# Optimization experiments

Measured on AMD Instinct MI355X. Metric: run time of the kernel, lower is better.

Reference implementation:

```python
import jax, jax.numpy as jnp
import numpy as np

N_NODES = 10000
N_EDGES = 640000
IN_CH = 128
OUT_CH = 128


def setup_inputs() -> dict:
    key = jax.random.key(0)
    k1, k2, k3, k4 = jax.random.split(key, 4)
    x = jax.random.normal(k1, (N_NODES, IN_CH), dtype=jnp.float32)
    edge_index = jax.random.randint(k2, (2, N_EDGES), 0, N_NODES, dtype=jnp.int64)
    # nn.Linear(2*in_channels, out_channels): weight [out, 2*in], bias [out]
    bound = 1.0 / np.sqrt(2 * IN_CH)
    W = jax.random.uniform(k3, (OUT_CH, 2 * IN_CH), dtype=jnp.float32, minval=-bound, maxval=bound)
    b = jax.random.uniform(k4, (OUT_CH,), dtype=jnp.float32, minval=-bound, maxval=bound)
    return {"x": x, "W": W, "b": b, "edge_index": edge_index}


def reference(x, W, b, edge_index):
    # PyG convention: edge_index[0] = source j, edge_index[1] = target i
    src, dst = edge_index[0], edge_index[1]
    x_i = x[dst]                      # [E, C] target features
    x_j = x[src]                      # [E, C] source features
    feat = jnp.concatenate([x_i, x_j - x_i], axis=-1)  # [E, 2C]
    msg = feat @ W.T + b              # [E, out]
    out = jax.ops.segment_max(msg, dst, num_segments=x.shape[0])  # [N, out]
    # isolated nodes: PyG scatter-max yields 0, segment_max yields -inf
    return jnp.where(jnp.isfinite(out), out, 0.0)
```

## Files before the change

### kernel.cpp

```cpp
#include <hip/hip_runtime.h>
#include <math.h>

#define N_CH 128
#define NB_MAX 512
#define BIN_CHUNK 2048
#define BIN_T 512

__global__ __launch_bounds__(256) void prep_kernel(const float* __restrict__ W,
                                                   float* __restrict__ V1,
                                                   float* __restrict__ V2,
                                                   int* __restrict__ binCount,
                                                   int nb) {
    int i = blockIdx.x * 256 + threadIdx.x;
    if (i < N_CH * N_CH) {
        int k = i >> 7, o = i & 127;
        float w1 = W[o * 256 + k];
        float w2 = W[o * 256 + 128 + k];
        V1[i] = w1 - w2;
        V2[i] = w2;
    }
    if (i < nb) binCount[i] = 0;
}

__global__ __launch_bounds__(256) void gemm_kernel(const float* __restrict__ x,
                                                   const float* __restrict__ V1,
                                                   const float* __restrict__ V2,
                                                   const float* __restrict__ bias,
                                                   float* __restrict__ A,
                                                   unsigned short* __restrict__ Bh,
                                                   int n_nodes) {
    __shared__ float xs[32][N_CH];
    const int n0 = blockIdx.x * 32;
    const int tid = threadIdx.x;

    if (n0 + 32 <= n_nodes) {
        const float4* xg = (const float4*)(x + (size_t)n0 * N_CH);
        float4* xsv = (float4*)&xs[0][0];
        #pragma unroll
        for (int i = 0; i < 4; ++i) xsv[tid + i * 256] = xg[tid + i * 256];
    } else {
        for (int i = tid; i < 32 * N_CH; i += 256) {
            int n = n0 + (i >> 7);
            (&xs[0][0])[i] = (n < n_nodes) ? x[(size_t)n * N_CH + (i & 127)] : 0.f;
        }
    }
    __syncthreads();

    const int o  = tid & 127;
    const int nh = tid >> 7;
    const float bo = bias[o];
    float acc1[16], acc2[16];
    #pragma unroll
    for (int i = 0; i < 16; ++i) { acc1[i] = 0.f; acc2[i] = 0.f; }

    const float* xrow = &xs[nh * 16][0];
    for (int k4 = 0; k4 < N_CH; k4 += 4) {
        float w1[4], w2[4];
        #pragma unroll
        for (int j = 0; j < 4; ++j) {
            w1[j] = V1[(k4 + j) * N_CH + o];
            w2[j] = V2[(k4 + j) * N_CH + o];
        }
        #pragma unroll
        for (int i = 0; i < 16; ++i) {
            float4 xv = *(const float4*)&xrow[i * N_CH + k4];
            acc1[i] = fmaf(xv.x, w1[0], acc1[i]); acc2[i] = fmaf(xv.x, w2[0], acc2[i]);
            acc1[i] = fmaf(xv.y, w1[1], acc1[i]); acc2[i] = fmaf(xv.y, w2[1], acc2[i]);
            acc1[i] = fmaf(xv.z, w1[2], acc1[i]); acc2[i] = fmaf(xv.z, w2[2], acc2[i]);
            acc1[i] = fmaf(xv.w, w1[3], acc1[i]); acc2[i] = fmaf(xv.w, w2[3], acc2[i]);
        }
    }

    #pragma unroll
    for (int i = 0; i < 16; ++i) {
        int n = n0 + nh * 16 + i;
        if (n < n_nodes) {
            A[(size_t)n * N_CH + o] = acc1[i] + bo;
            unsigned int bits = __float_as_uint(acc2[i]);
            unsigned int r = (bits + 0x7FFFu + ((bits >> 16) & 1u)) >> 16;
            Bh[(size_t)n * N_CH + o] = (unsigned short)r;
        }
    }
}

__global__ __launch_bounds__(256) void bhist_kernel(const int* __restrict__ dst,
                                                    int* __restrict__ binCount,
                                                    int n_edges, int nb) {
    __shared__ int h[NB_MAX];
    const int tid = threadIdx.x;
    for (int i = tid; i < nb; i += 256) h[i] = 0;
    __syncthreads();
    const int base = blockIdx.x * BIN_CHUNK;
    const int cnt = min(BIN_CHUNK, n_edges - base);
    for (int j = tid; j < cnt; j += 256)
        atomicAdd(&h[dst[base + j] >> 5], 1);
    __syncthreads();
    for (int i = tid; i < nb; i += 256)
        if (h[i]) atomicAdd(&binCount[i], h[i]);
}

__global__ __launch_bounds__(512) void bscan_kernel(const int* __restrict__ binCount,
                                                    int* __restrict__ binOff,
                                                    int* __restrict__ binCursor,
                                                    int nb) {
    __shared__ int t[512];
    const int tid = threadIdx.x;
    int v = (tid < nb) ? binCount[tid] : 0;
    t[tid] = v;
    __syncthreads();
    #pragma unroll
    for (int off = 1; off < 512; off <<= 1) {
        int u = (tid >= off) ? t[tid - off] : 0;
        __syncthreads();
        t[tid] += u;
        __syncthreads();
    }
    if (tid < nb) {
        int excl = t[tid] - v;
        binOff[tid] = excl;
        binCursor[tid] = excl;
    }
    if (tid == 0) binOff[nb] = t[nb - 1];
}

__global__ __launch_bounds__(BIN_T) void bin_kernel(const int* __restrict__ src,
                                                    const int* __restrict__ dst,
                                                    int* __restrict__ binCursor,
                                                    unsigned int* __restrict__ binned,
                                                    int n_edges, int nb) {
    __shared__ unsigned int   lpk[BIN_CHUNK];
    __shared__ unsigned short lbk[BIN_CHUNK];
    __shared__ int sc[512];
    __shared__ int lhist[NB_MAX], lexcl[NB_MAX], lcur[NB_MAX], bbase[NB_MAX];

    const int tid = threadIdx.x;
    const int base = blockIdx.x * BIN_CHUNK;
    const int cnt = min(BIN_CHUNK, n_edges - base);

    for (int i = tid; i < nb; i += BIN_T) lhist[i] = 0;
    __syncthreads();

    unsigned int vreg[BIN_CHUNK / BIN_T];
    unsigned short breg[BIN_CHUNK / BIN_T];
    int nloc = 0;
    for (int j = tid; j < cnt; j += BIN_T) {
        int s = src[base + j];
        int d = dst[base + j];
        int b = d >> 5;
        vreg[nloc] = ((unsigned int)(d & 31) << 14) | (unsigned int)s;
        breg[nloc] = (unsigned short)b;
        ++nloc;
        atomicAdd(&lhist[b], 1);
    }
    __syncthreads();

    int v = (tid < nb) ? lhist[tid] : 0;
    sc[tid] = v;
    __syncthreads();
    #pragma unroll
    for (int off = 1; off < 512; off <<= 1) {
        int u = (tid >= off) ? sc[tid - off] : 0;
        __syncthreads();
        sc[tid] += u;
        __syncthreads();
    }
    if (tid < nb) {
        int excl = sc[tid] - v;
        lexcl[tid] = excl;
        lcur[tid] = excl;
    }
    __syncthreads();

    for (int k = 0; k < nloc; ++k) {
        int b = breg[k];
        int p = atomicAdd(&lcur[b], 1);
        lpk[p] = vreg[k];
        lbk[p] = (unsigned short)b;
    }
    __syncthreads();

    for (int b = tid; b < nb; b += BIN_T) {
        int c = lhist[b];
        if (c) bbase[b] = atomicAdd(&binCursor[b], c);
    }
    __syncthreads();

    for (int i = tid; i < cnt; i += BIN_T) {
        int b = lbk[i];
        binned[bbase[b] + (i - lexcl[b])] = lpk[i];
    }
}

__global__ __launch_bounds__(256) void build_kernel(const unsigned int* __restrict__ binned,
                                                    const int* __restrict__ binOff,
                                                    int* __restrict__ offsets,
                                                    int* __restrict__ eidx,
                                                    int n_nodes, int nb) {
    __shared__ int lhist[32], lexcl[33], lcur[32];
    const int b = blockIdx.x;
    const int tid = threadIdx.x;
    const int rbeg = binOff[b], rend = binOff[b + 1];

    if (tid < 32) { lhist[tid] = 0; lcur[tid] = 0; }
    __syncthreads();
    for (int i = rbeg + tid; i < rend; i += 256)
        atomicAdd(&lhist[binned[i] >> 14], 1);
    __syncthreads();
    if (tid == 0) {
        int s = 0;
        for (int k = 0; k < 32; ++k) { lexcl[k] = s; s += lhist[k]; }
        lexcl[32] = s;
    }
    __syncthreads();
    if (tid < 32) {
        int n = b * 32 + tid;
        if (n < n_nodes) offsets[n] = rbeg + lexcl[tid];
    }
    if (b == nb - 1 && tid == 0) offsets[n_nodes] = rend;
    for (int i = rbeg + tid; i < rend; i += 256) {
        unsigned int w = binned[i];
        int d5 = (int)(w >> 14);
        int r = atomicAdd(&lcur[d5], 1);
        eidx[rbeg + lexcl[d5] + r] = (int)(w & 16383u);
    }
}

__global__ __launch_bounds__(256) void gather_kernel(
        const float* __restrict__ A,
        const uint4* __restrict__ Bh4,
        const int* __restrict__ offsets,
        const int* __restrict__ eidx,
        float* __restrict__ out,
        int n_nodes) {
    __shared__ int sidx[4][64];
    const int g = threadIdx.x >> 6;
    const int l = threadIdx.x & 63;
    const int n = blockIdx.x * 4 + g;
    if (n >= n_nodes) return;
    const int beg = offsets[n], end = offsets[n + 1];

    const int sub = l >> 4;
    const int col = l & 15;

    float mlo[4][4], mhi[4][4];
    #pragma unroll
    for (int s = 0; s < 4; ++s)
        #pragma unroll
        for (int u = 0; u < 4; ++u) { mlo[s][u] = -INFINITY; mhi[s][u] = -INFINITY; }

    for (int base = beg; base < end; base += 64) {
        int p = base + l;
        if (p < end) sidx[g][l] = eidx[p];
        int cnt = min(64, end - base);
        int q = 0;
        for (; q + 16 <= cnt; q += 16) {
            int e[4];
            #pragma unroll
            for (int s = 0; s < 4; ++s) e[s] = sidx[g][q + 4 * s + sub];
            uint4 w[4];
            #pragma unroll
            for (int s = 0; s < 4; ++s) w[s] = Bh4[(size_t)e[s] * 16 + col];
            #pragma unroll
            for (int s = 0; s < 4; ++s) {
                mlo[s][0] = fmaxf(mlo[s][0], __uint_as_float(w[s].x << 16));
                mhi[s][0] = fmaxf(mhi[s][0], __uint_as_float(w[s].x & 0xFFFF0000u));
                mlo[s][1] = fmaxf(mlo[s][1], __uint_as_float(w[s].y << 16));
                mhi[s][1] = fmaxf(mhi[s][1], __uint_as_float(w[s].y & 0xFFFF0000u));
                mlo[s][2] = fmaxf(mlo[s][2], __uint_as_float(w[s].z << 16));
                mhi[s][2] = fmaxf(mhi[s][2], __uint_as_float(w[s].z & 0xFFFF0000u));
                mlo[s][3] = fmaxf(mlo[s][3], __uint_as_float(w[s].w << 16));
                mhi[s][3] = fmaxf(mhi[s][3], __uint_as_float(w[s].w & 0xFFFF0000u));
            }
        }
        for (; q < cnt; q += 4) {
            int r = q + sub;
            if (r < cnt) {
                int e = sidx[g][r];
                uint4 w = Bh4[(size_t)e * 16 + col];
                mlo[0][0] = fmaxf(mlo[0][0], __uint_as_float(w.x << 16));
                mhi[0][0] = fmaxf(mhi[0][0], __uint_as_float(w.x & 0xFFFF0000u));
                mlo[0][1] = fmaxf(mlo[0][1], __uint_as_float(w.y << 16));
                mhi[0][1] = fmaxf(mhi[0][1], __uint_as_float(w.y & 0xFFFF0000u));
                mlo[0][2] = fmaxf(mlo[0][2], __uint_as_float(w.z << 16));
                mhi[0][2] = fmaxf(mhi[0][2], __uint_as_float(w.z & 0xFFFF0000u));
                mlo[0][3] = fmaxf(mlo[0][3], __uint_as_float(w.w << 16));
                mhi[0][3] = fmaxf(mhi[0][3], __uint_as_float(w.w & 0xFFFF0000u));
            }
        }
    }

    float lo[4], hi[4];
    #pragma unroll
    for (int u = 0; u < 4; ++u) {
        lo[u] = fmaxf(fmaxf(mlo[0][u], mlo[1][u]), fmaxf(mlo[2][u], mlo[3][u]));
        hi[u] = fmaxf(fmaxf(mhi[0][u], mhi[1][u]), fmaxf(mhi[2][u], mhi[3][u]));
    }
    #pragma unroll
    for (int u = 0; u < 4; ++u) {
        lo[u] = fmaxf(lo[u], __shfl_xor(lo[u], 16, 64));
        hi[u] = fmaxf(hi[u], __shfl_xor(hi[u], 16, 64));
        lo[u] = fmaxf(lo[u], __shfl_xor(lo[u], 32, 64));
        hi[u] = fmaxf(hi[u], __shfl_xor(hi[u], 32, 64));
    }

    if (sub == 0) {
        float r8[8];
        if (end > beg) {
            const float4* Arow = (const float4*)(A + (size_t)n * N_CH + col * 8);
            float4 a0 = Arow[0], a1 = Arow[1];
            r8[0] = a0.x + lo[0]; r8[1] = a0.y + hi[0];
            r8[2] = a0.z + lo[1]; r8[3] = a0.w + hi[1];
            r8[4] = a1.x + lo[2]; r8[5] = a1.y + hi[2];
            r8[6] = a1.z + lo[3]; r8[7] = a1.w + hi[3];
        } else {
            #pragma unroll
            for (int i = 0; i < 8; ++i) r8[i] = 0.f;
        }
        float4* orow = (float4*)(out + (size_t)n * N_CH + col * 8);
        orow[0] = make_float4(r8[0], r8[1], r8[2], r8[3]);
        orow[1] = make_float4(r8[4], r8[5], r8[6], r8[7]);
    }
}

extern "C" void kernel_launch(void* const* d_in, const int* in_sizes, int n_in,
                              void* d_out, int out_size, void* d_ws, size_t ws_size,
                              hipStream_t stream) {
    const float* x = (const float*)d_in[0];
    const float* W = (const float*)d_in[1];
    const float* b = (const float*)d_in[2];
    const int*   ei = (const int*)d_in[3];

    const int n_nodes = in_sizes[0] / N_CH;
    const int n_edges = in_sizes[3] / 2;
    const int nb = (n_nodes + 31) >> 5;
    const int* src = ei;
    const int* dst = ei + n_edges;
    float* out = (float*)d_out;

    char* ws = (char*)d_ws;
    size_t off = 0;
    auto alloc = [&](size_t bytes) -> void* {
        void* p = ws + off;
        off += (bytes + 255) & ~(size_t)255;
        return p;
    };
    float* V1        = (float*)alloc((size_t)N_CH * N_CH * 4);
    float* V2        = (float*)alloc((size_t)N_CH * N_CH * 4);
    float* A         = (float*)alloc((size_t)n_nodes * N_CH * 4);
    unsigned short* Bh = (unsigned short*)alloc((size_t)n_nodes * N_CH * 2);
    int*   binCount  = (int*)alloc((size_t)nb * 4);
    int*   binOff    = (int*)alloc((size_t)(nb + 1) * 4);
    int*   binCursor = (int*)alloc((size_t)nb * 4);
    unsigned int* binned = (unsigned int*)alloc((size_t)n_edges * 4);
    int*   offsets   = (int*)alloc((size_t)(n_nodes + 1) * 4);
    int*   eidx      = (int*)alloc((size_t)n_edges * 4);
    (void)ws_size; (void)n_in; (void)out_size;

    const int nbin_blocks = (n_edges + BIN_CHUNK - 1) / BIN_CHUNK;

    prep_kernel <<<(N_CH * N_CH + 255) / 256, 256, 0, stream>>>(W, V1, V2, binCount, nb);
    gemm_kernel <<<(n_nodes + 31) / 32, 256, 0, stream>>>(x, V1, V2, b, A, Bh, n_nodes);
    bhist_kernel<<<nbin_blocks, 256, 0, stream>>>(dst, binCount, n_edges, nb);
    bscan_kernel<<<1, 512, 0, stream>>>(binCount, binOff, binCursor, nb);
    bin_kernel  <<<nbin_blocks, BIN_T, 0, stream>>>(src, dst, binCursor, binned, n_edges, nb);
    build_kernel<<<nb, 256, 0, stream>>>(binned, binOff, offsets, eidx, n_nodes, nb);
    gather_kernel<<<(n_nodes + 3) / 4, 256, 0, stream>>>(A, (const uint4*)Bh, offsets, eidx, out, n_nodes);
}
```

Baseline: 141.9 us.

## Replace binned CSR build with per-node histogram fused into GEMM and atomic scatter

Removes the two-level bin/build CSR construction (bhist, bscan, bin, build kernels). A per-node degree histogram is now fused into the GEMM kernel, with a last-block-done pattern doing the prefix scan inside the same launch. A simple global-atomic scatter then fills eidx. This cuts launch count and intermediate traffic, but the scan now runs on a single block and the scatter uses contended global atomics. Edge order within each node also becomes nondeterministic, which is harmless for a max reduction.

```diff
diff --git a/kernel.cpp b/kernel.cpp
--- a/kernel.cpp
+++ b/kernel.cpp
@@ -2,15 +2,13 @@
 #include <math.h>
 
 #define N_CH 128
-#define NB_MAX 512
-#define BIN_CHUNK 2048
-#define BIN_T 512
 
 __global__ __launch_bounds__(256) void prep_kernel(const float* __restrict__ W,
                                                    float* __restrict__ V1,
                                                    float* __restrict__ V2,
-                                                   int* __restrict__ binCount,
-                                                   int nb) {
+                                                   int* __restrict__ nodeCount,
+                                                   int* __restrict__ done,
+                                                   int n_nodes) {
     int i = blockIdx.x * 256 + threadIdx.x;
     if (i < N_CH * N_CH) {
         int k = i >> 7, o = i & 127;
@@ -19,209 +17,143 @@
         V1[i] = w1 - w2;
         V2[i] = w2;
     }
-    if (i < nb) binCount[i] = 0;
-}
-
-__global__ __launch_bounds__(256) void gemm_kernel(const float* __restrict__ x,
-                                                   const float* __restrict__ V1,
-                                                   const float* __restrict__ V2,
-                                                   const float* __restrict__ bias,
-                                                   float* __restrict__ A,
-                                                   unsigned short* __restrict__ Bh,
-                                                   int n_nodes) {
-    __shared__ float xs[32][N_CH];
-    const int n0 = blockIdx.x * 32;
+    int total = gridDim.x * 256;
+    for (int j = i; j < n_nodes; j += total) nodeCount[j] = 0;
+    if (i == 0) *done = 0;
+}
+
+__global__ __launch_bounds__(256) void gemmhist_kernel(
+        const float* __restrict__ x,
+        const float* __restrict__ V1,
+        const float* __restrict__ V2,
+        const float* __restrict__ bias,
+        const int* __restrict__ dst,
+        float* __restrict__ A,
+        unsigned short* __restrict__ Bh,
+        int* __restrict__ nodeCount,
+        int* __restrict__ done,
+        int* __restrict__ offsets,
+        int* __restrict__ cursor,
+        int n_nodes, int n_edges, int ec) {
+    __shared__ float xs[16][N_CH];
+    __shared__ int ps[256];
+    __shared__ int isLast;
     const int tid = threadIdx.x;
-
-    if (n0 + 32 <= n_nodes) {
-        const float4* xg = (const float4*)(x + (size_t)n0 * N_CH);
-        float4* xsv = (float4*)&xs[0][0];
+    const int bid = blockIdx.x;
+
+    {
+        const int base = bid * ec;
+        const int cnt = min(ec, n_edges - base);
+        for (int j = tid; j < cnt; j += 256)
+            atomicAdd(&nodeCount[dst[base + j]], 1);
+    }
+
+    const int n0 = bid * 16;
+    if (n0 < n_nodes) {
+        if (n0 + 16 <= n_nodes) {
+            const float4* xg = (const float4*)(x + (size_t)n0 * N_CH);
+            float4* xsv = (float4*)&xs[0][0];
+            xsv[tid] = xg[tid];
+            xsv[tid + 256] = xg[tid + 256];
+        } else {
+            for (int i = tid; i < 16 * N_CH; i += 256) {
+                int n = n0 + (i >> 7);
+                (&xs[0][0])[i] = (n < n_nodes) ? x[(size_t)n * N_CH + (i & 127)] : 0.f;
+            }
+        }
+        __syncthreads();
+
+        const int o  = tid & 127;
+        const int nh = tid >> 7;
+        const float bo = bias[o];
+        float acc1[8], acc2[8];
         #pragma unroll
-        for (int i = 0; i < 4; ++i) xsv[tid + i * 256] = xg[tid + i * 256];
+        for (int i = 0; i < 8; ++i) { acc1[i] = 0.f; acc2[i] = 0.f; }
+
+        const float* xrow = &xs[nh * 8][0];
+        for (int k4 = 0; k4 < N_CH; k4 += 4) {
+            float w1[4], w2[4];
+            #pragma unroll
+            for (int j = 0; j < 4; ++j) {
+                w1[j] = V1[(k4 + j) * N_CH + o];
+                w2[j] = V2[(k4 + j) * N_CH + o];
+            }
+            #pragma unroll
+            for (int i = 0; i < 8; ++i) {
+                float4 xv = *(const float4*)&xrow[i * N_CH + k4];
+                acc1[i] = fmaf(xv.x, w1[0], acc1[i]); acc2[i] = fmaf(xv.x, w2[0], acc2[i]);
+                acc1[i] = fmaf(xv.y, w1[1], acc1[i]); acc2[i] = fmaf(xv.y, w2[1], acc2[i]);
+                acc1[i] = fmaf(xv.z, w1[2], acc1[i]); acc2[i] = fmaf(xv.z, w2[2], acc2[i]);
+                acc1[i] = fmaf(xv.w, w1[3], acc1[i]); acc2[i] = fmaf(xv.w, w2[3], acc2[i]);
+            }
+        }
+
+        #pragma unroll
+        for (int i = 0; i < 8; ++i) {
+            int n = n0 + nh * 8 + i;
+            if (n < n_nodes) {
+                A[(size_t)n * N_CH + o] = acc1[i] + bo;
+                unsigned int bits = __float_as_uint(acc2[i]);
+                unsigned int r = (bits + 0x7FFFu + ((bits >> 16) & 1u)) >> 16;
+                Bh[(size_t)n * N_CH + o] = (unsigned short)r;
+            }
+        }
+    }
+
+    __threadfence();
+    __syncthreads();
+    if (tid == 0) isLast = (atomicAdd(done, 1) == (int)gridDim.x - 1) ? 1 : 0;
+    __syncthreads();
+    if (!isLast) return;
+
+    const int npt = (n_nodes + 255) >> 8;
+    const int beg = tid * npt;
+    int s = 0;
+    for (int k = 0; k < npt; ++k) {
+        int idx = beg + k;
+        if (idx < n_nodes) s += atomicAdd(&nodeCount[idx], 0);
+    }
+    ps[tid] = s;
+    __syncthreads();
+    #pragma unroll
+    for (int off = 1; off < 256; off <<= 1) {
+        int u = (tid >= off) ? ps[tid - off] : 0;
+        __syncthreads();
+        ps[tid] += u;
+        __syncthreads();
+    }
+    int run = ps[tid] - s;
+    for (int k = 0; k < npt; ++k) {
+        int idx = beg + k;
+        if (idx < n_nodes) {
+            int c = atomicAdd(&nodeCount[idx], 0);
+            offsets[idx] = run;
+            cursor[idx]  = run;
+            run += c;
+        }
+    }
+    if (tid == 255) offsets[n_nodes] = ps[255];
+}
+
+__global__ __launch_bounds__(256) void scatter_kernel(const int* __restrict__ src,
+                                                      const int* __restrict__ dst,
+                                                      int* __restrict__ cursor,
+                                                      int* __restrict__ eidx,
+                                                      int n_edges) {
+    const int g = blockIdx.x * 256 + threadIdx.x;
+    const int base = g * 4;
+    if (base + 4 <= n_edges) {
+        int4 s4 = *(const int4*)(src + base);
+        int4 d4 = *(const int4*)(dst + base);
+        int p0 = atomicAdd(&cursor[d4.x], 1); eidx[p0] = s4.x;
+        int p1 = atomicAdd(&cursor[d4.y], 1); eidx[p1] = s4.y;
+        int p2 = atomicAdd(&cursor[d4.z], 1); eidx[p2] = s4.z;
+        int p3 = atomicAdd(&cursor[d4.w], 1); eidx[p3] = s4.w;
     } else {
-        for (int i = tid; i < 32 * N_CH; i += 256) {
-            int n = n0 + (i >> 7);
-            (&xs[0][0])[i] = (n < n_nodes) ? x[(size_t)n * N_CH + (i & 127)] : 0.f;
-        }
-    }
-    __syncthreads();
-
-    const int o  = tid & 127;
-    const int nh = tid >> 7;
-    const float bo = bias[o];
-    float acc1[16], acc2[16];
-    #pragma unroll
-    for (int i = 0; i < 16; ++i) { acc1[i] = 0.f; acc2[i] = 0.f; }
-
-    const float* xrow = &xs[nh * 16][0];
-    for (int k4 = 0; k4 < N_CH; k4 += 4) {
-        float w1[4], w2[4];
-        #pragma unroll
-        for (int j = 0; j < 4; ++j) {
-            w1[j] = V1[(k4 + j) * N_CH + o];
-            w2[j] = V2[(k4 + j) * N_CH + o];
-        }
-        #pragma unroll
-        for (int i = 0; i < 16; ++i) {
-            float4 xv = *(const float4*)&xrow[i * N_CH + k4];
-            acc1[i] = fmaf(xv.x, w1[0], acc1[i]); acc2[i] = fmaf(xv.x, w2[0], acc2[i]);
-            acc1[i] = fmaf(xv.y, w1[1], acc1[i]); acc2[i] = fmaf(xv.y, w2[1], acc2[i]);
-            acc1[i] = fmaf(xv.z, w1[2], acc1[i]); acc2[i] = fmaf(xv.z, w2[2], acc2[i]);
-            acc1[i] = fmaf(xv.w, w1[3], acc1[i]); acc2[i] = fmaf(xv.w, w2[3], acc2[i]);
-        }
-    }
-
-    #pragma unroll
-    for (int i = 0; i < 16; ++i) {
-        int n = n0 + nh * 16 + i;
-        if (n < n_nodes) {
-            A[(size_t)n * N_CH + o] = acc1[i] + bo;
-            unsigned int bits = __float_as_uint(acc2[i]);
-            unsigned int r = (bits + 0x7FFFu + ((bits >> 16) & 1u)) >> 16;
-            Bh[(size_t)n * N_CH + o] = (unsigned short)r;
-        }
-    }
-}
-
-__global__ __launch_bounds__(256) void bhist_kernel(const int* __restrict__ dst,
-                                                    int* __restrict__ binCount,
-                                                    int n_edges, int nb) {
-    __shared__ int h[NB_MAX];
-    const int tid = threadIdx.x;
-    for (int i = tid; i < nb; i += 256) h[i] = 0;
-    __syncthreads();
-    const int base = blockIdx.x * BIN_CHUNK;
-    const int cnt = min(BIN_CHUNK, n_edges - base);
-    for (int j = tid; j < cnt; j += 256)
-        atomicAdd(&h[dst[base + j] >> 5], 1);
-    __syncthreads();
-    for (int i = tid; i < nb; i += 256)
-        if (h[i]) atomicAdd(&binCount[i], h[i]);
-}
-
-__global__ __launch_bounds__(512) void bscan_kernel(const int* __restrict__ binCount,
-                                                    int* __restrict__ binOff,
-                                                    int* __restrict__ binCursor,
-                                                    int nb) {
-    __shared__ int t[512];
-    const int tid = threadIdx.x;
-    int v = (tid < nb) ? binCount[tid] : 0;
-    t[tid] = v;
-    __syncthreads();
-    #pragma unroll
-    for (int off = 1; off < 512; off <<= 1) {
-        int u = (tid >= off) ? t[tid - off] : 0;
-        __syncthreads();
-        t[tid] += u;
-        __syncthreads();
-    }
-    if (tid < nb) {
-        int excl = t[tid] - v;
-        binOff[tid] = excl;
-        binCursor[tid] = excl;
-    }
-    if (tid == 0) binOff[nb] = t[nb - 1];
-}
-
-__global__ __launch_bounds__(BIN_T) void bin_kernel(const int* __restrict__ src,
-                                                    const int* __restrict__ dst,
-                                                    int* __restrict__ binCursor,
-                                                    unsigned int* __restrict__ binned,
-                                                    int n_edges, int nb) {
-    __shared__ unsigned int   lpk[BIN_CHUNK];
-    __shared__ unsigned short lbk[BIN_CHUNK];
-    __shared__ int sc[512];
-    __shared__ int lhist[NB_MAX], lexcl[NB_MAX], lcur[NB_MAX], bbase[NB_MAX];
-
-    const int tid = threadIdx.x;
-    const int base = blockIdx.x * BIN_CHUNK;
-    const int cnt = min(BIN_CHUNK, n_edges - base);
-
-    for (int i = tid; i < nb; i += BIN_T) lhist[i] = 0;
-    __syncthreads();
-
-    unsigned int vreg[BIN_CHUNK / BIN_T];
-    unsigned short breg[BIN_CHUNK / BIN_T];
-    int nloc = 0;
-    for (int j = tid; j < cnt; j += BIN_T) {
-        int s = src[base + j];
-        int d = dst[base + j];
-        int b = d >> 5;
-        vreg[nloc] = ((unsigned int)(d & 31) << 14) | (unsigned int)s;
-        breg[nloc] = (unsigned short)b;
-        ++nloc;
-        atomicAdd(&lhist[b], 1);
-    }
-    __syncthreads();
-
-    int v = (tid < nb) ? lhist[tid] : 0;
-    sc[tid] = v;
-    __syncthreads();
-    #pragma unroll
-    for (int off = 1; off < 512; off <<= 1) {
-        int u = (tid >= off) ? sc[tid - off] : 0;
-        __syncthreads();
-        sc[tid] += u;
-        __syncthreads();
-    }
-    if (tid < nb) {
-        int excl = sc[tid] - v;
-        lexcl[tid] = excl;
-        lcur[tid] = excl;
-    }
-    __syncthreads();
-
-    for (int k = 0; k < nloc; ++k) {
-        int b = breg[k];
-        int p = atomicAdd(&lcur[b], 1);
-        lpk[p] = vreg[k];
-        lbk[p] = (unsigned short)b;
-    }
-    __syncthreads();
-
-    for (int b = tid; b < nb; b += BIN_T) {
-        int c = lhist[b];
-        if (c) bbase[b] = atomicAdd(&binCursor[b], c);
-    }
-    __syncthreads();
-
-    for (int i = tid; i < cnt; i += BIN_T) {
-        int b = lbk[i];
-        binned[bbase[b] + (i - lexcl[b])] = lpk[i];
-    }
-}
-
-__global__ __launch_bounds__(256) void build_kernel(const unsigned int* __restrict__ binned,
-                                                    const int* __restrict__ binOff,
-                                                    int* __restrict__ offsets,
-                                                    int* __restrict__ eidx,
-                                                    int n_nodes, int nb) {
-    __shared__ int lhist[32], lexcl[33], lcur[32];
-    const int b = blockIdx.x;
-    const int tid = threadIdx.x;
-    const int rbeg = binOff[b], rend = binOff[b + 1];
-
-    if (tid < 32) { lhist[tid] = 0; lcur[tid] = 0; }
-    __syncthreads();
-    for (int i = rbeg + tid; i < rend; i += 256)
-        atomicAdd(&lhist[binned[i] >> 14], 1);
-    __syncthreads();
-    if (tid == 0) {
-        int s = 0;
-        for (int k = 0; k < 32; ++k) { lexcl[k] = s; s += lhist[k]; }
-        lexcl[32] = s;
-    }
-    __syncthreads();
-    if (tid < 32) {
-        int n = b * 32 + tid;
-        if (n < n_nodes) offsets[n] = rbeg + lexcl[tid];
-    }
-    if (b == nb - 1 && tid == 0) offsets[n_nodes] = rend;
-    for (int i = rbeg + tid; i < rend; i += 256) {
-        unsigned int w = binned[i];
-        int d5 = (int)(w >> 14);
-        int r = atomicAdd(&lcur[d5], 1);
-        eidx[rbeg + lexcl[d5] + r] = (int)(w & 16383u);
+        for (int j = base; j < n_edges; ++j) {
+            int p = atomicAdd(&cursor[dst[j]], 1);
+            eidx[p] = src[j];
+        }
     }
 }
 
@@ -332,7 +264,6 @@
 
     const int n_nodes = in_sizes[0] / N_CH;
     const int n_edges = in_sizes[3] / 2;
-    const int nb = (n_nodes + 31) >> 5;
     const int* src = ei;
     const int* dst = ei + n_edges;
     float* out = (float*)d_out;
@@ -348,21 +279,20 @@
     float* V2        = (float*)alloc((size_t)N_CH * N_CH * 4);
     float* A         = (float*)alloc((size_t)n_nodes * N_CH * 4);
     unsigned short* Bh = (unsigned short*)alloc((size_t)n_nodes * N_CH * 2);
-    int*   binCount  = (int*)alloc((size_t)nb * 4);
-    int*   binOff    = (int*)alloc((size_t)(nb + 1) * 4);
-    int*   binCursor = (int*)alloc((size_t)nb * 4);
-    unsigned int* binned = (unsigned int*)alloc((size_t)n_edges * 4);
+    int*   nodeCount = (int*)alloc((size_t)n_nodes * 4);
+    int*   done      = (int*)alloc(256);
     int*   offsets   = (int*)alloc((size_t)(n_nodes + 1) * 4);
+    int*   cursor    = (int*)alloc((size_t)n_nodes * 4);
     int*   eidx      = (int*)alloc((size_t)n_edges * 4);
     (void)ws_size; (void)n_in; (void)out_size;
 
-    const int nbin_blocks = (n_edges + BIN_CHUNK - 1) / BIN_CHUNK;
-
-    prep_kernel <<<(N_CH * N_CH + 255) / 256, 256, 0, stream>>>(W, V1, V2, binCount, nb);
-    gemm_kernel <<<(n_nodes + 31) / 32, 256, 0, stream>>>(x, V1, V2, b, A, Bh, n_nodes);
-    bhist_kernel<<<nbin_blocks, 256, 0, stream>>>(dst, binCount, n_edges, nb);
-    bscan_kernel<<<1, 512, 0, stream>>>(binCount, binOff, binCursor, nb);
-    bin_kernel  <<<nbin_blocks, BIN_T, 0, stream>>>(src, dst, binCursor, binned, n_edges, nb);
-    build_kernel<<<nb, 256, 0, stream>>>(binned, binOff, offsets, eidx, n_nodes, nb);
-    gather_kernel<<<(n_nodes + 3) / 4, 256, 0, stream>>>(A, (const uint4*)Bh, offsets, eidx, out, n_nodes);
-}
+    const int ng = (n_nodes + 15) / 16;
+    const int ec = (n_edges + ng - 1) / ng;
+    const int ns = (n_edges + 1023) / 1024;
+
+    prep_kernel   <<<64, 256, 0, stream>>>(W, V1, V2, nodeCount, done, n_nodes);
+    gemmhist_kernel<<<ng, 256, 0, stream>>>(x, V1, V2, b, dst, A, Bh, nodeCount, done,
+                                            offsets, cursor, n_nodes, n_edges, ec);
+    scatter_kernel<<<ns, 256, 0, stream>>>(src, dst, cursor, eidx, n_edges);
+    gather_kernel <<<(n_nodes + 3) / 4, 256, 0, stream>>>(A, (const uint4*)Bh, offsets, eidx, out, n_nodes);
+}
```

Result: slower. 262.1 us (+84.7%).

## Fuse edge histogram into GEMM, fold scan into binning, build CSR in gather

Applied to the files above, without the earlier changes.

Merges the destination histogram into the GEMM kernel, moves the bin prefix scan into every bin block (with padded bin offsets), and removes the per-node CSR build pass by having the gather kernel sort each 32-node bin in shared memory before reducing. This cuts the launch count from seven to four and drops the eidx/offsets round trip through global memory. In exchange every bin block recomputes the scan redundantly, gather blocks now do local counting-sort work, and the binned order of edges within a bin is nondeterministic.

```diff
diff --git a/kernel.cpp b/kernel.cpp
--- a/kernel.cpp
+++ b/kernel.cpp
@@ -3,13 +3,14 @@
 
 #define N_CH 128
 #define NB_MAX 512
-#define BIN_CHUNK 2048
-#define BIN_T 512
+#define ECHUNK 2048
+#define GCHUNK 2048
 
 __global__ __launch_bounds__(256) void prep_kernel(const float* __restrict__ W,
                                                    float* __restrict__ V1,
                                                    float* __restrict__ V2,
                                                    int* __restrict__ binCount,
+                                                   int* __restrict__ binCursor,
                                                    int nb) {
     int i = blockIdx.x * 256 + threadIdx.x;
     if (i < N_CH * N_CH) {
@@ -19,19 +20,47 @@
         V1[i] = w1 - w2;
         V2[i] = w2;
     }
-    if (i < nb) binCount[i] = 0;
+    if (i < nb) { binCount[i] = 0; binCursor[i] = 0; }
 }
 
 __global__ __launch_bounds__(256) void gemm_kernel(const float* __restrict__ x,
                                                    const float* __restrict__ V1,
                                                    const float* __restrict__ V2,
                                                    const float* __restrict__ bias,
+                                                   const int* __restrict__ dst,
                                                    float* __restrict__ A,
                                                    unsigned short* __restrict__ Bh,
-                                                   int n_nodes) {
+                                                   int* __restrict__ binCount,
+                                                   int n_nodes, int n_edges, int nb) {
     __shared__ float xs[32][N_CH];
-    const int n0 = blockIdx.x * 32;
+    __shared__ int h[NB_MAX];
     const int tid = threadIdx.x;
+    const int bid = blockIdx.x;
+
+    const int ebase = bid * ECHUNK;
+    const int ecnt = min(ECHUNK, n_edges - ebase);
+    for (int i = tid; i < nb; i += 256) h[i] = 0;
+    __syncthreads();
+    if (ecnt > 0) {
+        const int j = tid * 8;
+        if (j + 8 <= ecnt) {
+            int4 d0 = *(const int4*)(dst + ebase + j);
+            int4 d1 = *(const int4*)(dst + ebase + j + 4);
+            atomicAdd(&h[d0.x >> 5], 1); atomicAdd(&h[d0.y >> 5], 1);
+            atomicAdd(&h[d0.z >> 5], 1); atomicAdd(&h[d0.w >> 5], 1);
+            atomicAdd(&h[d1.x >> 5], 1); atomicAdd(&h[d1.y >> 5], 1);
+            atomicAdd(&h[d1.z >> 5], 1); atomicAdd(&h[d1.w >> 5], 1);
+        } else {
+            for (int q = j; q < min(j + 8, ecnt); ++q)
+                atomicAdd(&h[dst[ebase + q] >> 5], 1);
+        }
+    }
+    __syncthreads();
+    for (int i = tid; i < nb; i += 256)
+        if (h[i]) atomicAdd(&binCount[i], h[i]);
+
+    const int n0 = bid * 32;
+    if (n0 >= n_nodes) return;
 
     if (n0 + 32 <= n_nodes) {
         const float4* xg = (const float4*)(x + (size_t)n0 * N_CH);
@@ -83,242 +112,224 @@
     }
 }
 
-__global__ __launch_bounds__(256) void bhist_kernel(const int* __restrict__ dst,
-                                                    int* __restrict__ binCount,
-                                                    int n_edges, int nb) {
-    __shared__ int h[NB_MAX];
+__global__ __launch_bounds__(256) void bin_kernel(const int* __restrict__ src,
+                                                  const int* __restrict__ dst,
+                                                  const int* __restrict__ binCount,
+                                                  int* __restrict__ binCursor,
+                                                  int* __restrict__ binOffG,
+                                                  unsigned int* __restrict__ binned,
+                                                  int n_edges, int nb) {
+    __shared__ int sc[512];
+    __shared__ int bOff[512];
     const int tid = threadIdx.x;
-    for (int i = tid; i < nb; i += 256) h[i] = 0;
-    __syncthreads();
-    const int base = blockIdx.x * BIN_CHUNK;
-    const int cnt = min(BIN_CHUNK, n_edges - base);
-    for (int j = tid; j < cnt; j += 256)
-        atomicAdd(&h[dst[base + j] >> 5], 1);
-    __syncthreads();
-    for (int i = tid; i < nb; i += 256)
-        if (h[i]) atomicAdd(&binCount[i], h[i]);
-}
-
-__global__ __launch_bounds__(512) void bscan_kernel(const int* __restrict__ binCount,
-                                                    int* __restrict__ binOff,
-                                                    int* __restrict__ binCursor,
-                                                    int nb) {
-    __shared__ int t[512];
-    const int tid = threadIdx.x;
-    int v = (tid < nb) ? binCount[tid] : 0;
-    t[tid] = v;
+    const int base = blockIdx.x * ECHUNK;
+    const int cnt = min(ECHUNK, n_edges - base);
+
+    int c0 = (tid < nb) ? binCount[tid] : 0;
+    int c1 = (tid + 256 < nb) ? binCount[tid + 256] : 0;
+    int p0 = (c0 + 3) & ~3, p1 = (c1 + 3) & ~3;
+    sc[tid] = p0; sc[tid + 256] = p1;
     __syncthreads();
     #pragma unroll
     for (int off = 1; off < 512; off <<= 1) {
-        int u = (tid >= off) ? t[tid - off] : 0;
-        __syncthreads();
-        t[tid] += u;
-        __syncthreads();
-    }
-    if (tid < nb) {
-        int excl = t[tid] - v;
-        binOff[tid] = excl;
-        binCursor[tid] = excl;
-    }
-    if (tid == 0) binOff[nb] = t[nb - 1];
-}
-
-__global__ __launch_bounds__(BIN_T) void bin_kernel(const int* __restrict__ src,
-                                                    const int* __restrict__ dst,
-                                                    int* __restrict__ binCursor,
-                                                    unsigned int* __restrict__ binned,
-                                                    int n_edges, int nb) {
-    __shared__ unsigned int   lpk[BIN_CHUNK];
-    __shared__ unsigned short lbk[BIN_CHUNK];
-    __shared__ int sc[512];
-    __shared__ int lhist[NB_MAX], lexcl[NB_MAX], lcur[NB_MAX], bbase[NB_MAX];
-
-    const int tid = threadIdx.x;
-    const int base = blockIdx.x * BIN_CHUNK;
-    const int cnt = min(BIN_CHUNK, n_edges - base);
-
-    for (int i = tid; i < nb; i += BIN_T) lhist[i] = 0;
-    __syncthreads();
-
-    unsigned int vreg[BIN_CHUNK / BIN_T];
-    unsigned short breg[BIN_CHUNK / BIN_T];
-    int nloc = 0;
-    for (int j = tid; j < cnt; j += BIN_T) {
-        int s = src[base + j];
-        int d = dst[base + j];
-        int b = d >> 5;
-        vreg[nloc] = ((unsigned int)(d & 31) << 14) | (unsigned int)s;
-        breg[nloc] = (unsigned short)b;
-        ++nloc;
-        atomicAdd(&lhist[b], 1);
-    }
-    __syncthreads();
-
-    int v = (tid < nb) ? lhist[tid] : 0;
-    sc[tid] = v;
-    __syncthreads();
-    #pragma unroll
-    for (int off = 1; off < 512; off <<= 1) {
-        int u = (tid >= off) ? sc[tid - off] : 0;
-        __syncthreads();
-        sc[tid] += u;
-        __syncthreads();
-    }
-    if (tid < nb) {
-        int excl = sc[tid] - v;
-        lexcl[tid] = excl;
-        lcur[tid] = excl;
-    }
-    __syncthreads();
-
-    for (int k = 0; k < nloc; ++k) {
-        int b = breg[k];
-        int p = atomicAdd(&lcur[b], 1);
-        lpk[p] = vreg[k];
-        lbk[p] = (unsigned short)b;
-    }
-    __syncthreads();
-
-    for (int b = tid; b < nb; b += BIN_T) {
-        int c = lhist[b];
-        if (c) bbase[b] = atomicAdd(&binCursor[b], c);
-    }
-    __syncthreads();
-
-    for (int i = tid; i < cnt; i += BIN_T) {
-        int b = lbk[i];
-        binned[bbase[b] + (i - lexcl[b])] = lpk[i];
-    }
-}
-
-__global__ __launch_bounds__(256) void build_kernel(const unsigned int* __restrict__ binned,
-                                                    const int* __restrict__ binOff,
-                                                    int* __restrict__ offsets,
-                                                    int* __restrict__ eidx,
-                                                    int n_nodes, int nb) {
-    __shared__ int lhist[32], lexcl[33], lcur[32];
+        int u0 = (tid >= off) ? sc[tid - off] : 0;
+        int u1 = sc[tid + 256 - off];
+        __syncthreads();
+        sc[tid] += u0; sc[tid + 256] += u1;
+        __syncthreads();
+    }
+    bOff[tid] = sc[tid] - p0;
+    bOff[tid + 256] = sc[tid + 256] - p1;
+    if (blockIdx.x == 0) {
+        if (tid < nb) binOffG[tid] = bOff[tid];
+        if (tid + 256 < nb) binOffG[tid + 256] = bOff[tid + 256];
+    }
+    sc[tid] = 0; sc[tid + 256] = 0;
+    __syncthreads();
+
+    const int myb = tid * 8;
+    const int mycnt = max(0, min(8, cnt - myb));
+    unsigned int pk[8]; int bb[8], rr[8];
+    if (mycnt == 8) {
+        int4 s0 = *(const int4*)(src + base + myb);
+        int4 s1 = *(const int4*)(src + base + myb + 4);
+        int4 d0 = *(const int4*)(dst + base + myb);
+        int4 d1 = *(const int4*)(dst + base + myb + 4);
+        int sv[8] = {s0.x, s0.y, s0.z, s0.w, s1.x, s1.y, s1.z, s1.w};
+        int dv[8] = {d0.x, d0.y, d0.z, d0.w, d1.x, d1.y, d1.z, d1.w};
+        #pragma unroll
+        for (int k = 0; k < 8; ++k) {
+            int b = dv[k] >> 5;
+            pk[k] = ((unsigned int)(dv[k] & 31) << 14) | (unsigned int)sv[k];
+            bb[k] = b;
+            rr[k] = atomicAdd(&sc[b], 1);
+        }
+    } else {
+        for (int k = 0; k < mycnt; ++k) {
+            int s = src[base + myb + k];
+            int d = dst[base + myb + k];
+            int b = d >> 5;
+            pk[k] = ((unsigned int)(d & 31) << 14) | (unsigned int)s;
+            bb[k] = b;
+            rr[k] = atomicAdd(&sc[b], 1);
+        }
+    }
+    __syncthreads();
+
+    for (int i = tid; i < nb; i += 256) {
+        int c = sc[i];
+        if (c) bOff[i] += atomicAdd(&binCursor[i], c);
+    }
+    __syncthreads();
+
+    for (int k = 0; k < mycnt; ++k)
+        binned[bOff[bb[k]] + rr[k]] = pk[k];
+}
+
+#define FOLD4(acc_lo, acc_hi, a, b, c, d)                                        \
+    acc_lo = fmaxf(acc_lo, fmaxf(fmaxf(__uint_as_float((a) << 16),               \
+                                       __uint_as_float((b) << 16)),              \
+                                 fmaxf(__uint_as_float((c) << 16),               \
+                                       __uint_as_float((d) << 16))));            \
+    acc_hi = fmaxf(acc_hi, fmaxf(fmaxf(__uint_as_float((a) & 0xFFFF0000u),       \
+                                       __uint_as_float((b) & 0xFFFF0000u)),      \
+                                 fmaxf(__uint_as_float((c) & 0xFFFF0000u),       \
+                                       __uint_as_float((d) & 0xFFFF0000u))));
+
+__global__ __launch_bounds__(512) void gather_kernel(
+        const float* __restrict__ A,
+        const uint4* __restrict__ Bh4,
+        const int* __restrict__ binOffG,
+        const int* __restrict__ binCount,
+        const unsigned int* __restrict__ binned,
+        float* __restrict__ out,
+        int n_nodes) {
+    __shared__ int lidx[GCHUNK];
+    __shared__ int h32[32], e33[33];
     const int b = blockIdx.x;
     const int tid = threadIdx.x;
-    const int rbeg = binOff[b], rend = binOff[b + 1];
-
-    if (tid < 32) { lhist[tid] = 0; lcur[tid] = 0; }
-    __syncthreads();
-    for (int i = rbeg + tid; i < rend; i += 256)
-        atomicAdd(&lhist[binned[i] >> 14], 1);
-    __syncthreads();
-    if (tid == 0) {
-        int s = 0;
-        for (int k = 0; k < 32; ++k) { lexcl[k] = s; s += lhist[k]; }
-        lexcl[32] = s;
-    }
-    __syncthreads();
-    if (tid < 32) {
-        int n = b * 32 + tid;
-        if (n < n_nodes) offsets[n] = rbeg + lexcl[tid];
-    }
-    if (b == nb - 1 && tid == 0) offsets[n_nodes] = rend;
-    for (int i = rbeg + tid; i < rend; i += 256) {
-        unsigned int w = binned[i];
-        int d5 = (int)(w >> 14);
-        int r = atomicAdd(&lcur[d5], 1);
-        eidx[rbeg + lexcl[d5] + r] = (int)(w & 16383u);
-    }
-}
-
-__global__ __launch_bounds__(256) void gather_kernel(
-        const float* __restrict__ A,
-        const uint4* __restrict__ Bh4,
-        const int* __restrict__ offsets,
-        const int* __restrict__ eidx,
-        float* __restrict__ out,
-        int n_nodes) {
-    __shared__ int sidx[4][64];
-    const int g = threadIdx.x >> 6;
-    const int l = threadIdx.x & 63;
-    const int n = blockIdx.x * 4 + g;
-    if (n >= n_nodes) return;
-    const int beg = offsets[n], end = offsets[n + 1];
-
+    const int wv  = tid >> 6;
+    const int l   = tid & 63;
     const int sub = l >> 4;
     const int col = l & 15;
-
-    float mlo[4][4], mhi[4][4];
-    #pragma unroll
-    for (int s = 0; s < 4; ++s)
-        #pragma unroll
-        for (int u = 0; u < 4; ++u) { mlo[s][u] = -INFINITY; mhi[s][u] = -INFINITY; }
-
-    for (int base = beg; base < end; base += 64) {
-        int p = base + l;
-        if (p < end) sidx[g][l] = eidx[p];
-        int cnt = min(64, end - base);
-        int q = 0;
-        for (; q + 16 <= cnt; q += 16) {
-            int e[4];
+    const int rbeg = binOffG[b];
+    const int cnt  = binCount[b];
+
+    float mlo[4][4], mhi[4][4]; int tcnt[4];
+    #pragma unroll
+    for (int i = 0; i < 4; ++i) {
+        tcnt[i] = 0;
+        #pragma unroll
+        for (int u = 0; u < 4; ++u) { mlo[i][u] = -INFINITY; mhi[i][u] = -INFINITY; }
+    }
+
+    for (int cb = 0; cb < cnt; cb += GCHUNK) {
+        const int ccnt = min(GCHUNK, cnt - cb);
+        if (tid < 32) h32[tid] = 0;
+        __syncthreads();
+
+        const int mb = tid * 4;
+        const int mc = max(0, min(4, ccnt - mb));
+        int myd[4], mys[4], myr[4];
+        if (mc == 4) {
+            int4 r4 = *(const int4*)((const int*)binned + rbeg + cb + mb);
+            unsigned int wv4[4] = {(unsigned int)r4.x, (unsigned int)r4.y,
+                                   (unsigned int)r4.z, (unsigned int)r4.w};
             #pragma unroll
-            for (int s = 0; s < 4; ++s) e[s] = sidx[g][q + 4 * s + sub];
-            uint4 w[4];
+            for (int k = 0; k < 4; ++k) {
+                myd[k] = (int)(wv4[k] >> 14);
+                mys[k] = (int)(wv4[k] & 16383u);
+                myr[k] = atomicAdd(&h32[myd[k]], 1);
+            }
+        } else {
+            for (int k = 0; k < mc; ++k) {
+                unsigned int w = binned[rbeg + cb + mb + k];
+                myd[k] = (int)(w >> 14);
+                mys[k] = (int)(w & 16383u);
+                myr[k] = atomicAdd(&h32[myd[k]], 1);
+            }
+        }
+        __syncthreads();
+        if (tid == 0) {
+            int s = 0;
             #pragma unroll
-            for (int s = 0; s < 4; ++s) w[s] = Bh4[(size_t)e[s] * 16 + col];
-            #pragma unroll
-            for (int s = 0; s < 4; ++s) {
-                mlo[s][0] = fmaxf(mlo[s][0], __uint_as_float(w[s].x << 16));
-                mhi[s][0] = fmaxf(mhi[s][0], __uint_as_float(w[s].x & 0xFFFF0000u));
-                mlo[s][1] = fmaxf(mlo[s][1], __uint_as_float(w[s].y << 16));
-                mhi[s][1] = fmaxf(mhi[s][1], __uint_as_float(w[s].y & 0xFFFF0000u));
-                mlo[s][2] = fmaxf(mlo[s][2], __uint_as_float(w[s].z << 16));
-                mhi[s][2] = fmaxf(mhi[s][2], __uint_as_float(w[s].z & 0xFFFF0000u));
-                mlo[s][3] = fmaxf(mlo[s][3], __uint_as_float(w[s].w << 16));
-                mhi[s][3] = fmaxf(mhi[s][3], __uint_as_float(w[s].w & 0xFFFF0000u));
-            }
-        }
-        for (; q < cnt; q += 4) {
-            int r = q + sub;
-            if (r < cnt) {
-                int e = sidx[g][r];
-                uint4 w = Bh4[(size_t)e * 16 + col];
-                mlo[0][0] = fmaxf(mlo[0][0], __uint_as_float(w.x << 16));
-                mhi[0][0] = fmaxf(mhi[0][0], __uint_as_float(w.x & 0xFFFF0000u));
-                mlo[0][1] = fmaxf(mlo[0][1], __uint_as_float(w.y << 16));
-                mhi[0][1] = fmaxf(mhi[0][1], __uint_as_float(w.y & 0xFFFF0000u));
-                mlo[0][2] = fmaxf(mlo[0][2], __uint_as_float(w.z << 16));
-                mhi[0][2] = fmaxf(mhi[0][2], __uint_as_float(w.z & 0xFFFF0000u));
-                mlo[0][3] = fmaxf(mlo[0][3], __uint_as_float(w.w << 16));
-                mhi[0][3] = fmaxf(mhi[0][3], __uint_as_float(w.w & 0xFFFF0000u));
-            }
-        }
-    }
-
-    float lo[4], hi[4];
-    #pragma unroll
-    for (int u = 0; u < 4; ++u) {
-        lo[u] = fmaxf(fmaxf(mlo[0][u], mlo[1][u]), fmaxf(mlo[2][u], mlo[3][u]));
-        hi[u] = fmaxf(fmaxf(mhi[0][u], mhi[1][u]), fmaxf(mhi[2][u], mhi[3][u]));
-    }
-    #pragma unroll
-    for (int u = 0; u < 4; ++u) {
-        lo[u] = fmaxf(lo[u], __shfl_xor(lo[u], 16, 64));
-        hi[u] = fmaxf(hi[u], __shfl_xor(hi[u], 16, 64));
-        lo[u] = fmaxf(lo[u], __shfl_xor(lo[u], 32, 64));
-        hi[u] = fmaxf(hi[u], __shfl_xor(hi[u], 32, 64));
-    }
-
-    if (sub == 0) {
-        float r8[8];
-        if (end > beg) {
-            const float4* Arow = (const float4*)(A + (size_t)n * N_CH + col * 8);
-            float4 a0 = Arow[0], a1 = Arow[1];
-            r8[0] = a0.x + lo[0]; r8[1] = a0.y + hi[0];
-            r8[2] = a0.z + lo[1]; r8[3] = a0.w + hi[1];
-            r8[4] = a1.x + lo[2]; r8[5] = a1.y + hi[2];
-            r8[6] = a1.z + lo[3]; r8[7] = a1.w + hi[3];
-        } else {
-            #pragma unroll
-            for (int i = 0; i < 8; ++i) r8[i] = 0.f;
-        }
-        float4* orow = (float4*)(out + (size_t)n * N_CH + col * 8);
-        orow[0] = make_float4(r8[0], r8[1], r8[2], r8[3]);
-        orow[1] = make_float4(r8[4], r8[5], r8[6], r8[7]);
+            for (int k = 0; k < 32; ++k) { e33[k] = s; s += h32[k]; }
+            e33[32] = s;
+        }
+        __syncthreads();
+        for (int k = 0; k < mc; ++k)
+            lidx[e33[myd[k]] + myr[k]] = mys[k];
+        __syncthreads();
+
+        #pragma unroll
+        for (int i = 0; i < 4; ++i) {
+            const int nl = wv * 4 + i;
+            const int c  = h32[nl];
+            const int bg = e33[nl];
+            tcnt[i] += c;
+            int q = 0;
+            for (; q + 16 <= c; q += 16) {
+                int e0 = lidx[bg + q + sub];
+                int e1 = lidx[bg + q + 4 + sub];
+                int e2 = lidx[bg + q + 8 + sub];
+                int e3 = lidx[bg + q + 12 + sub];
+                uint4 w0 = Bh4[(size_t)e0 * 16 + col];
+                uint4 w1 = Bh4[(size_t)e1 * 16 + col];
+                uint4 w2 = Bh4[(size_t)e2 * 16 + col];
+                uint4 w3 = Bh4[(size_t)e3 * 16 + col];
+                FOLD4(mlo[i][0], mhi[i][0], w0.x, w1.x, w2.x, w3.x);
+                FOLD4(mlo[i][1], mhi[i][1], w0.y, w1.y, w2.y, w3.y);
+                FOLD4(mlo[i][2], mhi[i][2], w0.z, w1.z, w2.z, w3.z);
+                FOLD4(mlo[i][3], mhi[i][3], w0.w, w1.w, w2.w, w3.w);
+            }
+            for (; q < c; q += 4) {
+                int r = q + sub;
+                if (r < c) {
+                    uint4 w = Bh4[(size_t)lidx[bg + r] * 16 + col];
+                    mlo[i][0] = fmaxf(mlo[i][0], __uint_as_float(w.x << 16));
+                    mhi[i][0] = fmaxf(mhi[i][0], __uint_as_float(w.x & 0xFFFF0000u));
+                    mlo[i][1] = fmaxf(mlo[i][1], __uint_as_float(w.y << 16));
+                    mhi[i][1] = fmaxf(mhi[i][1], __uint_as_float(w.y & 0xFFFF0000u));
+                    mlo[i][2] = fmaxf(mlo[i][2], __uint_as_float(w.z << 16));
+                    mhi[i][2] = fmaxf(mhi[i][2], __uint_as_float(w.z & 0xFFFF0000u));
+                    mlo[i][3] = fmaxf(mlo[i][3], __uint_as_float(w.w << 16));
+                    mhi[i][3] = fmaxf(mhi[i][3], __uint_as_float(w.w & 0xFFFF0000u));
+                }
+            }
+        }
+        __syncthreads();
+    }
+
+    #pragma unroll
+    for (int i = 0; i < 4; ++i) {
+        const int n = b * 32 + wv * 4 + i;
+        if (n >= n_nodes) continue;
+        float lo[4], hi[4];
+        #pragma unroll
+        for (int u = 0; u < 4; ++u) {
+            lo[u] = mlo[i][u]; hi[u] = mhi[i][u];
+            lo[u] = fmaxf(lo[u], __shfl_xor(lo[u], 16, 64));
+            hi[u] = fmaxf(hi[u], __shfl_xor(hi[u], 16, 64));
+            lo[u] = fmaxf(lo[u], __shfl_xor(lo[u], 32, 64));
+            hi[u] = fmaxf(hi[u], __shfl_xor(hi[u], 32, 64));
+        }
+        if (sub == 0) {
+            float r8[8];
+            if (tcnt[i] > 0) {
+                const float4* Arow = (const float4*)(A + (size_t)n * N_CH + col * 8);
+                float4 a0 = Arow[0], a1 = Arow[1];
+                r8[0] = a0.x + lo[0]; r8[1] = a0.y + hi[0];
+                r8[2] = a0.z + lo[1]; r8[3] = a0.w + hi[1];
+                r8[4] = a1.x + lo[2]; r8[5] = a1.y + hi[2];
+                r8[6] = a1.z + lo[3]; r8[7] = a1.w + hi[3];
+            } else {
+                #pragma unroll
+                for (int j = 0; j < 8; ++j) r8[j] = 0.f;
+            }
+            float4* orow = (float4*)(out + (size_t)n * N_CH + col * 8);
+            orow[0] = make_float4(r8[0], r8[1], r8[2], r8[3]);
+            orow[1] = make_float4(r8[4], r8[5], r8[6], r8[7]);
+        }
     }
 }
 
@@ -349,20 +360,20 @@
     float* A         = (float*)alloc((size_t)n_nodes * N_CH * 4);
     unsigned short* Bh = (unsigned short*)alloc((size_t)n_nodes * N_CH * 2);
     int*   binCount  = (int*)alloc((size_t)nb * 4);
-    int*   binOff    = (int*)alloc((size_t)(nb + 1) * 4);
     int*   binCursor = (int*)alloc((size_t)nb * 4);
-    unsigned int* binned = (unsigned int*)alloc((size_t)n_edges * 4);
-    int*   offsets   = (int*)alloc((size_t)(n_nodes + 1) * 4);
-    int*   eidx      = (int*)alloc((size_t)n_edges * 4);
+    int*   binOffG   = (int*)alloc((size_t)nb * 4);
+    unsigned int* binned = (unsigned int*)alloc(((size_t)n_edges + 4 * NB_MAX) * 4);
     (void)ws_size; (void)n_in; (void)out_size;
 
-    const int nbin_blocks = (n_edges + BIN_CHUNK - 1) / BIN_CHUNK;
-
-    prep_kernel <<<(N_CH * N_CH + 255) / 256, 256, 0, stream>>>(W, V1, V2, binCount, nb);
-    gemm_kernel <<<(n_nodes + 31) / 32, 256, 0, stream>>>(x, V1, V2, b, A, Bh, n_nodes);
-    bhist_kernel<<<nbin_blocks, 256, 0, stream>>>(dst, binCount, n_edges, nb);
-    bscan_kernel<<<1, 512, 0, stream>>>(binCount, binOff, binCursor, nb);
-    bin_kernel  <<<nbin_blocks, BIN_T, 0, stream>>>(src, dst, binCursor, binned, n_edges, nb);
-    build_kernel<<<nb, 256, 0, stream>>>(binned, binOff, offsets, eidx, n_nodes, nb);
-    gather_kernel<<<(n_nodes + 3) / 4, 256, 0, stream>>>(A, (const uint4*)Bh, offsets, eidx, out, n_nodes);
-}
+    const int nodeBlocks = (n_nodes + 31) / 32;
+    const int edgeBlocks = (n_edges + ECHUNK - 1) / ECHUNK;
+    const int ng = max(nodeBlocks, edgeBlocks);
+
+    prep_kernel  <<<64, 256, 0, stream>>>(W, V1, V2, binCount, binCursor, nb);
+    gemm_kernel  <<<ng, 256, 0, stream>>>(x, V1, V2, b, dst, A, Bh, binCount,
+                                          n_nodes, n_edges, nb);
+    bin_kernel   <<<edgeBlocks, 256, 0, stream>>>(src, dst, binCount, binCursor,
+                                                  binOffG, binned, n_edges, nb);
+    gather_kernel<<<nb, 512, 0, stream>>>(A, (const uint4*)Bh, binOffG, binCount,
+                                          binned, out, n_nodes);
+}
```

Result: faster. 136.6 us (-3.8%).
